# Kernel tuning notes

Measured on AMD Instinct MI355X. Metric: run time of the kernel, lower is better.

## Reference

```python
import jax, jax.numpy as jnp
import numpy as np
from jax import lax

E, H, D = 1024, 16, 64          # embed_dim, num_heads, head_dim
B, T = 8, 64                    # batch, decode chunk
KV = 4096                       # kv_seq_len -> cache capacity 2*KV
START = 4096                    # start_pos (prefill already filled cache[:START])
THETA = 10000.0


def setup_inputs() -> dict:
    key = jax.random.key(0)
    kx, kck, kcv, kq, kk, kv, ko = jax.random.split(key, 7)
    s = 0.02
    return {
        "x": jax.random.normal(kx, (B, T, E), jnp.float32),
        "cache_keys": jax.random.normal(kck, (B, 2 * KV, H, D), jnp.float32),
        "cache_values": jax.random.normal(kcv, (B, 2 * KV, H, D), jnp.float32),
        "Wq": jax.random.normal(kq, (E, E), jnp.float32) * s,
        "Wk": jax.random.normal(kk, (E, E), jnp.float32) * s,
        "Wv": jax.random.normal(kv, (E, E), jnp.float32) * s,
        "Wo": jax.random.normal(ko, (E, E), jnp.float32) * s,
        "start_pos": START,
    }


def _rope_bug_faithful(x, start_pos):
    # x: (B, T, H, Dd). The source helper unpacks (B,H,T,D)=x.shape on a (B,T,H,D)
    # tensor, so rotation angles are indexed by HEAD index (positions
    # start_pos..start_pos+H-1) and broadcast over the time axis. Reproduced exactly.
    Bn, Tn, Hn, Dd = x.shape
    dh = Dd // 2
    inv_freq = 1.0 / (THETA ** (jnp.arange(dh, dtype=jnp.float32) / dh))
    pos = jnp.arange(Hn, dtype=jnp.float32) + jnp.float32(start_pos)  # (H,)
    ang = pos[:, None] * inv_freq[None, :]                            # (H, dh)
    cos = jnp.cos(ang)[None, None]                                    # (1,1,H,dh)
    sin = jnp.sin(ang)[None, None]
    xr = x.reshape(Bn, Tn, Hn, dh, 2)
    x0, x1 = xr[..., 0], xr[..., 1]
    o0 = x0 * cos - x1 * sin
    o1 = x0 * sin + x1 * cos
    return jnp.stack([o0, o1], axis=-1).reshape(Bn, Tn, Hn, Dd)


def reference(x, cache_keys, cache_values, Wq, Wk, Wv, Wo, start_pos):
    Bn, Tn, C = x.shape
    Hn, Dd = cache_keys.shape[2], cache_keys.shape[3]
    scale = 1.0 / np.sqrt(Dd).astype(np.float32)
    end = start_pos + Tn

    q = (x @ Wq).reshape(Bn, Tn, Hn, Dd)
    k = (x @ Wk).reshape(Bn, Tn, Hn, Dd)
    v = (x @ Wv).reshape(Bn, Tn, Hn, Dd)

    q = _rope_bug_faithful(q, start_pos)
    k = _rope_bug_faithful(k, start_pos)

    # cache append at dynamic offset (detached in source)
    ck = lax.dynamic_update_slice_in_dim(cache_keys, lax.stop_gradient(k), start_pos, axis=1)
    cv = lax.dynamic_update_slice_in_dim(cache_values, lax.stop_gradient(v), start_pos, axis=1)
    k_full = lax.stop_gradient(ck[:, :end])  # (B, S, H, D), S = end
    v_full = lax.stop_gradient(cv[:, :end])

    qh = q.transpose(0, 2, 1, 3)        # (B,H,T,D)
    kh = k_full.transpose(0, 2, 1, 3)   # (B,H,S,D)
    vh = v_full.transpose(0, 2, 1, 3)

    scores = jnp.einsum("bhtd,bhsd->bhts", qh, kh) * scale  # (B,H,T,S)
    i = jnp.arange(Tn)[:, None]
    j = jnp.arange(end)[None, :]
    allowed = j <= (start_pos + i)      # intended causal mask over cache span
    neg = jnp.finfo(scores.dtype).min
    scores = jnp.where(allowed[None, None], scores, neg)
    attn = jax.nn.softmax(scores, axis=-1)
    ctx = jnp.einsum("bhts,bhsd->bhtd", attn, vh)
    out = ctx.transpose(0, 2, 1, 3).reshape(Bn, Tn, C) @ Wo
    return out
```

## Files before the change

kernel.cpp:

```cpp
#include <hip/hip_runtime.h>
#include <hip/hip_bf16.h>
#include <math.h>

typedef __attribute__((ext_vector_type(8))) __bf16 bf16x8;
typedef __attribute__((ext_vector_type(4))) __bf16 bf16x4;
typedef __attribute__((ext_vector_type(4))) float f32x4;

#define EE 1024
#define HH 16
#define DD 64
#define BB 8
#define TT 64
#define NSPLIT 8

__device__ __forceinline__ f32x4 mfma16(bf16x8 a, bf16x8 b, f32x4 c) {
    return __builtin_amdgcn_mfma_f32_16x16x32_bf16(a, b, c, 0, 0, 0);
}

__global__ __launch_bounds__(256) void k_prep(const float* __restrict__ Wq, const float* __restrict__ Wk,
                                              const float* __restrict__ Wv, const float* __restrict__ Wo,
                                              const float* __restrict__ x, const int* __restrict__ sp_ptr,
                                              __bf16* __restrict__ WT, __bf16* __restrict__ xb,
                                              float* __restrict__ cs, float* __restrict__ sn) {
    __shared__ float tile[64][68];
    int bid = blockIdx.x;
    int tid = threadIdx.x;
    if (bid < 1024) {
        int w = bid >> 8, tl = bid & 255;
        int k0 = (tl >> 4) * 64, n0 = (tl & 15) * 64;
        const float* W = (w == 0) ? Wq : (w == 1) ? Wk : (w == 2) ? Wv : Wo;
#pragma unroll
        for (int p = 0; p < 4; ++p) {
            int idx = p * 256 + tid;
            int r = idx >> 4, c4 = (idx & 15) * 4;
            float4 f = *(const float4*)&W[(size_t)(k0 + r) * EE + n0 + c4];
            *(float4*)&tile[r][c4] = f;
        }
        __syncthreads();
        __bf16* out = WT + (size_t)w * EE * EE;
#pragma unroll
        for (int p = 0; p < 2; ++p) {
            int q = p * 256 + tid;
            int r = q >> 3, c8 = (q & 7) * 8;
            bf16x8 v;
#pragma unroll
            for (int j = 0; j < 8; ++j) v[j] = (__bf16)tile[c8 + j][r];
            *(bf16x8*)&out[(size_t)(n0 + r) * EE + k0 + c8] = v;
        }
    } else if (bid < 1280) {
        int i = ((bid - 1024) * 256 + tid) * 8;
        float4 a = *(const float4*)&x[i];
        float4 b = *(const float4*)&x[i + 4];
        bf16x8 v;
        v[0] = (__bf16)a.x; v[1] = (__bf16)a.y; v[2] = (__bf16)a.z; v[3] = (__bf16)a.w;
        v[4] = (__bf16)b.x; v[5] = (__bf16)b.y; v[6] = (__bf16)b.z; v[7] = (__bf16)b.w;
        *(bf16x8*)&xb[i] = v;
    } else {
        int sp = sp_ptr[0];
#pragma unroll
        for (int q = 0; q < 2; ++q) {
            int i = q * 256 + tid;
            int h = i >> 5, p = i & 31;
            double inv = 1.0 / pow(10000.0, (double)p / 32.0);
            double ang = (double)(sp + h) * inv;
            cs[i] = (float)cos(ang);
            sn[i] = (float)sin(ang);
        }
    }
}

__global__ __launch_bounds__(256) void k_qkv(const __bf16* __restrict__ xb, const __bf16* __restrict__ WT,
                                             const float* __restrict__ cs, const float* __restrict__ sn,
                                             __bf16* __restrict__ qws, __bf16* __restrict__ knew,
                                             __bf16* __restrict__ vnew) {
    __shared__ __bf16 a_lds[64][72];
    __shared__ __bf16 b_lds[64][72];
    int xcd = blockIdx.x & 7, idx = blockIdx.x >> 3;
    int bn = xcd * 6 + idx % 6;
    int bm = idx / 6;
    int wsel = bn >> 4;
    int n0 = (bn & 15) * 64;
    int m0 = bm * 64;
    const __bf16* Wt = WT + (size_t)wsel * EE * EE;
    int tid = threadIdx.x;
    int wv = tid >> 6, lane = tid & 63;
    int l16 = lane & 15, lhi = lane >> 4;
    int r0 = tid >> 3, c8 = (tid & 7) * 8;

    f32x4 acc[4];
#pragma unroll
    for (int f = 0; f < 4; ++f) acc[f] = (f32x4){0.f, 0.f, 0.f, 0.f};

    bf16x8 ar0 = *(const bf16x8*)&xb[(size_t)(m0 + r0) * EE + c8];
    bf16x8 ar1 = *(const bf16x8*)&xb[(size_t)(m0 + 32 + r0) * EE + c8];
    bf16x8 br0 = *(const bf16x8*)&Wt[(size_t)(n0 + r0) * EE + c8];
    bf16x8 br1 = *(const bf16x8*)&Wt[(size_t)(n0 + 32 + r0) * EE + c8];

    for (int kt = 0; kt < 16; ++kt) {
        __syncthreads();
        *(bf16x8*)&a_lds[r0][c8] = ar0;
        *(bf16x8*)&a_lds[32 + r0][c8] = ar1;
        *(bf16x8*)&b_lds[r0][c8] = br0;
        *(bf16x8*)&b_lds[32 + r0][c8] = br1;
        if (kt < 15) {
            int ko = (kt + 1) * 64;
            ar0 = *(const bf16x8*)&xb[(size_t)(m0 + r0) * EE + ko + c8];
            ar1 = *(const bf16x8*)&xb[(size_t)(m0 + 32 + r0) * EE + ko + c8];
            br0 = *(const bf16x8*)&Wt[(size_t)(n0 + r0) * EE + ko + c8];
            br1 = *(const bf16x8*)&Wt[(size_t)(n0 + 32 + r0) * EE + ko + c8];
        }
        __syncthreads();
        bf16x8 a0 = *(bf16x8*)&a_lds[wv * 16 + l16][lhi * 8];
        bf16x8 a1 = *(bf16x8*)&a_lds[wv * 16 + l16][32 + lhi * 8];
#pragma unroll
        for (int f = 0; f < 4; ++f) {
            bf16x8 b0 = *(bf16x8*)&b_lds[f * 16 + l16][lhi * 8];
            bf16x8 b1 = *(bf16x8*)&b_lds[f * 16 + l16][32 + lhi * 8];
            acc[f] = mfma16(a0, b0, acc[f]);
            acc[f] = mfma16(a1, b1, acc[f]);
        }
    }
    __bf16* dst = (wsel == 0) ? qws : (wsel == 1) ? knew : vnew;
#pragma unroll
    for (int f = 0; f < 4; ++f) {
#pragma unroll
        for (int r = 0; r < 4; ++r) {
            float v = acc[f][r];
            int row = m0 + wv * 16 + lhi * 4 + r;
            int ng = n0 + f * 16 + l16;
            int h = ng >> 6, d = ng & 63;
            float o = v;
            if (wsel < 2) {
                float other = __shfl_xor(v, 1);
                int pp = d >> 1;
                float c = cs[h * 32 + pp], s = sn[h * 32 + pp];
                o = ((d & 1) == 0) ? (v * c - other * s) : (other * s + v * c);
            }
            int b = row >> 6, t = row & 63;
            dst[((size_t)((b * HH + h) * TT + t)) * DD + d] = (__bf16)o;
        }
    }
}

__global__ __launch_bounds__(256, 4) void k_attn(const __bf16* __restrict__ qws, const __bf16* __restrict__ knew,
                                                 const __bf16* __restrict__ vnew,
                                                 const float* __restrict__ ck, const float* __restrict__ cv,
                                                 __bf16* __restrict__ Opart, float2* __restrict__ mlpart) {
    __shared__ __bf16 k_lds[64][72];
    __shared__ __bf16 vT_lds[64][68];
    __shared__ __bf16 p_lds[64][72];
    int bh = blockIdx.x >> 3, split = blockIdx.x & 7;
    int b = bh >> 4, h = bh & 15;
    int tid = threadIdx.x, wv = tid >> 6, lane = tid & 63;
    int l16 = lane & 15, lhi = lane >> 4;
    int g = tid >> 4, m4 = (tid & 15) * 4;

    bf16x8 qf0, qf1;
    {
        const __bf16* qp = qws + ((size_t)bh * TT + (wv * 16 + l16)) * DD;
        qf0 = *(const bf16x8*)&qp[lhi * 8];
        qf1 = *(const bf16x8*)&qp[32 + lhi * 8];
    }
    f32x4 acc[4];
#pragma unroll
    for (int f = 0; f < 4; ++f) acc[f] = (f32x4){0.f, 0.f, 0.f, 0.f};
    float m[4], l[4];
#pragma unroll
    for (int r = 0; r < 4; ++r) { m[r] = -1e30f; l[r] = 0.f; }

    const float* ckb = ck + (size_t)b * 8192 * EE + h * DD;
    const float* cvb = cv + (size_t)b * 8192 * EE + h * DD;
    int s0 = split * 512;

    auto compute = [&](bool mask) {
        f32x4 sf[4];
#pragma unroll
        for (int f = 0; f < 4; ++f) {
            f32x4 z = (f32x4){0.f, 0.f, 0.f, 0.f};
            bf16x8 b0 = *(bf16x8*)&k_lds[f * 16 + l16][lhi * 8];
            bf16x8 b1 = *(bf16x8*)&k_lds[f * 16 + l16][32 + lhi * 8];
            z = mfma16(qf0, b0, z);
            z = mfma16(qf1, b1, z);
            sf[f] = z;
        }
#pragma unroll
        for (int f = 0; f < 4; ++f) {
#pragma unroll
            for (int r = 0; r < 4; ++r) {
                float sv = sf[f][r] * 0.125f;
                if (mask) {
                    int t_row = wv * 16 + lhi * 4 + r;
                    int s_loc = f * 16 + l16;
                    if (s_loc > t_row) sv = -1e30f;
                }
                sf[f][r] = sv;
            }
        }
        float mt[4];
#pragma unroll
        for (int r = 0; r < 4; ++r)
            mt[r] = fmaxf(fmaxf(sf[0][r], sf[1][r]), fmaxf(sf[2][r], sf[3][r]));
#pragma unroll
        for (int off = 1; off < 16; off <<= 1) {
#pragma unroll
            for (int r = 0; r < 4; ++r) mt[r] = fmaxf(mt[r], __shfl_xor(mt[r], off));
        }
        float fac[4];
#pragma unroll
        for (int r = 0; r < 4; ++r) {
            float mn = fmaxf(m[r], mt[r]);
            fac[r] = __expf(m[r] - mn);
            m[r] = mn;
        }
        float ladd[4] = {0.f, 0.f, 0.f, 0.f};
#pragma unroll
        for (int f = 0; f < 4; ++f) {
#pragma unroll
            for (int r = 0; r < 4; ++r) {
                float pv = __expf(sf[f][r] - m[r]);
                sf[f][r] = pv;
                ladd[r] += pv;
            }
        }
#pragma unroll
        for (int off = 1; off < 16; off <<= 1) {
#pragma unroll
            for (int r = 0; r < 4; ++r) ladd[r] += __shfl_xor(ladd[r], off);
        }
#pragma unroll
        for (int r = 0; r < 4; ++r) l[r] = l[r] * fac[r] + ladd[r];
#pragma unroll
        for (int f = 0; f < 4; ++f)
#pragma unroll
            for (int r = 0; r < 4; ++r) acc[f][r] *= fac[r];
#pragma unroll
        for (int f = 0; f < 4; ++f)
#pragma unroll
            for (int r = 0; r < 4; ++r)
                p_lds[wv * 16 + lhi * 4 + r][f * 16 + l16] = (__bf16)sf[f][r];
        bf16x8 pa0 = *(bf16x8*)&p_lds[wv * 16 + l16][lhi * 8];
        bf16x8 pa1 = *(bf16x8*)&p_lds[wv * 16 + l16][32 + lhi * 8];
#pragma unroll
        for (int f = 0; f < 4; ++f) {
            bf16x8 v0 = *(bf16x8*)&vT_lds[f * 16 + l16][lhi * 8];
            bf16x8 v1 = *(bf16x8*)&vT_lds[f * 16 + l16][32 + lhi * 8];
            acc[f] = mfma16(pa0, v0, acc[f]);
            acc[f] = mfma16(pa1, v1, acc[f]);
        }
    };

    f32x4 kreg[4], vreg[4];
#pragma unroll
    for (int p = 0; p < 4; ++p)
        kreg[p] = *(const f32x4*)&ckb[(size_t)(s0 + p * 16 + g) * EE + m4];
#pragma unroll
    for (int i = 0; i < 4; ++i)
        vreg[i] = *(const f32x4*)&cvb[(size_t)(s0 + 4 * g + i) * EE + m4];

    for (int it = 0; it < 8; ++it) {
#pragma unroll
        for (int p = 0; p < 4; ++p) {
            bf16x4 k4 = { (__bf16)kreg[p][0], (__bf16)kreg[p][1], (__bf16)kreg[p][2], (__bf16)kreg[p][3] };
            *(bf16x4*)&k_lds[p * 16 + g][m4] = k4;
        }
#pragma unroll
        for (int j = 0; j < 4; ++j) {
            bf16x4 tv = { (__bf16)vreg[0][j], (__bf16)vreg[1][j], (__bf16)vreg[2][j], (__bf16)vreg[3][j] };
            *(bf16x4*)&vT_lds[m4 + j][4 * g] = tv;
        }
        if (it < 7) {
            int sb = s0 + (it + 1) * 64;
#pragma unroll
            for (int p = 0; p < 4; ++p)
                kreg[p] = *(const f32x4*)&ckb[(size_t)(sb + p * 16 + g) * EE + m4];
#pragma unroll
            for (int i = 0; i < 4; ++i)
                vreg[i] = *(const f32x4*)&cvb[(size_t)(sb + 4 * g + i) * EE + m4];
        }
        __syncthreads();
        compute(false);
        __syncthreads();
    }

    if (split == 7) {
#pragma unroll
        for (int p = 0; p < 2; ++p) {
            int idx = p * 256 + tid;
            int r = idx >> 3, c8 = (idx & 7) * 8;
            *(bf16x8*)&k_lds[r][c8] = *(const bf16x8*)&knew[((size_t)bh * TT + r) * DD + c8];
            bf16x8 vf = *(const bf16x8*)&vnew[((size_t)bh * TT + r) * DD + c8];
#pragma unroll
            for (int j = 0; j < 8; ++j) vT_lds[c8 + j][r] = vf[j];
        }
        __syncthreads();
        compute(true);
    }

#pragma unroll
    for (int f = 0; f < 4; ++f)
#pragma unroll
        for (int r = 0; r < 4; ++r) {
            int t = wv * 16 + lhi * 4 + r;
            int d = f * 16 + l16;
            Opart[(((size_t)split * 128 + bh) * TT + t) * DD + d] = (__bf16)acc[f][r];
        }
    if (l16 == 0) {
#pragma unroll
        for (int r = 0; r < 4; ++r) {
            int t = wv * 16 + lhi * 4 + r;
            mlpart[((size_t)split * 128 + bh) * TT + t] = make_float2(m[r], l[r]);
        }
    }
}

__global__ __launch_bounds__(256) void k_combine(const __bf16* __restrict__ Opart, const float2* __restrict__ mlpart,
                                                 __bf16* __restrict__ ctxb) {
    int idx = blockIdx.x * 256 + threadIdx.x;
    int d = idx & 63, t = (idx >> 6) & 63, bh = idx >> 12;
    float ms[NSPLIT], ls[NSPLIT];
    float mg = -1e30f;
#pragma unroll
    for (int s = 0; s < NSPLIT; ++s) {
        float2 ml = mlpart[((size_t)s * 128 + bh) * TT + t];
        ms[s] = ml.x; ls[s] = ml.y;
        mg = fmaxf(mg, ms[s]);
    }
    float den = 0.f, num = 0.f;
#pragma unroll
    for (int s = 0; s < NSPLIT; ++s) {
        float w = __expf(ms[s] - mg);
        den += ls[s] * w;
        num += (float)Opart[(((size_t)s * 128 + bh) * TT + t) * DD + d] * w;
    }
    float ctx = num / den;
    int b = bh >> 4, hh = bh & 15;
    ctxb[(size_t)(b * TT + t) * EE + hh * DD + d] = (__bf16)ctx;
}

__global__ __launch_bounds__(256) void k_oproj(const __bf16* __restrict__ ctxb, const __bf16* __restrict__ WoT,
                                               float* __restrict__ out) {
    __shared__ __bf16 a_lds[64][72];
    __shared__ __bf16 b_lds[64][72];
    int xcd = blockIdx.x & 7, idx = blockIdx.x >> 3;
    int bn = xcd * 2 + (idx & 1);
    int bm = idx >> 1;
    int n0 = bn * 64, m0 = bm * 64;
    int tid = threadIdx.x;
    int wv = tid >> 6, lane = tid & 63;
    int l16 = lane & 15, lhi = lane >> 4;
    int r0 = tid >> 3, c8 = (tid & 7) * 8;
    f32x4 acc[4];
#pragma unroll
    for (int f = 0; f < 4; ++f) acc[f] = (f32x4){0.f, 0.f, 0.f, 0.f};

    bf16x8 ar0 = *(const bf16x8*)&ctxb[(size_t)(m0 + r0) * EE + c8];
    bf16x8 ar1 = *(const bf16x8*)&ctxb[(size_t)(m0 + 32 + r0) * EE + c8];
    bf16x8 br0 = *(const bf16x8*)&WoT[(size_t)(n0 + r0) * EE + c8];
    bf16x8 br1 = *(const bf16x8*)&WoT[(size_t)(n0 + 32 + r0) * EE + c8];

    for (int kt = 0; kt < 16; ++kt) {
        __syncthreads();
        *(bf16x8*)&a_lds[r0][c8] = ar0;
        *(bf16x8*)&a_lds[32 + r0][c8] = ar1;
        *(bf16x8*)&b_lds[r0][c8] = br0;
        *(bf16x8*)&b_lds[32 + r0][c8] = br1;
        if (kt < 15) {
            int ko = (kt + 1) * 64;
            ar0 = *(const bf16x8*)&ctxb[(size_t)(m0 + r0) * EE + ko + c8];
            ar1 = *(const bf16x8*)&ctxb[(size_t)(m0 + 32 + r0) * EE + ko + c8];
            br0 = *(const bf16x8*)&WoT[(size_t)(n0 + r0) * EE + ko + c8];
            br1 = *(const bf16x8*)&WoT[(size_t)(n0 + 32 + r0) * EE + ko + c8];
        }
        __syncthreads();
        bf16x8 a0 = *(bf16x8*)&a_lds[wv * 16 + l16][lhi * 8];
        bf16x8 a1 = *(bf16x8*)&a_lds[wv * 16 + l16][32 + lhi * 8];
#pragma unroll
        for (int f = 0; f < 4; ++f) {
            bf16x8 b0 = *(bf16x8*)&b_lds[f * 16 + l16][lhi * 8];
            bf16x8 b1 = *(bf16x8*)&b_lds[f * 16 + l16][32 + lhi * 8];
            acc[f] = mfma16(a0, b0, acc[f]);
            acc[f] = mfma16(a1, b1, acc[f]);
        }
    }
#pragma unroll
    for (int f = 0; f < 4; ++f)
#pragma unroll
        for (int r = 0; r < 4; ++r) {
            int row = m0 + wv * 16 + lhi * 4 + r;
            out[(size_t)row * EE + n0 + f * 16 + l16] = acc[f][r];
        }
}

extern "C" void kernel_launch(void* const* d_in, const int* in_sizes, int n_in,
                              void* d_out, int out_size, void* d_ws, size_t ws_size,
                              hipStream_t stream) {
    const float* x  = (const float*)d_in[0];
    const float* ck = (const float*)d_in[1];
    const float* cv = (const float*)d_in[2];
    const float* Wq = (const float*)d_in[3];
    const float* Wk = (const float*)d_in[4];
    const float* Wv = (const float*)d_in[5];
    const float* Wo = (const float*)d_in[6];
    const int* sp   = (const int*)d_in[7];
    float* out = (float*)d_out;

    char* p = (char*)d_ws;
    float* cs = (float*)p;              p += 2048;
    float* sn = (float*)p;              p += 2048;
    __bf16* xb = (__bf16*)p;            p += (size_t)512 * 1024 * 2;
    __bf16* WT = (__bf16*)p;            p += (size_t)4 * 1024 * 1024 * 2;
    __bf16* qws = (__bf16*)p;           p += (size_t)524288 * 2;
    __bf16* knew = (__bf16*)p;          p += (size_t)524288 * 2;
    __bf16* vnew = (__bf16*)p;          p += (size_t)524288 * 2;
    __bf16* Opart = (__bf16*)p;         p += (size_t)NSPLIT * 128 * 64 * 64 * 2;
    float2* mlpart = (float2*)p;        p += (size_t)NSPLIT * 8192 * 8;
    __bf16* ctxb = (__bf16*)p;          p += (size_t)524288 * 2;

    k_prep<<<1281, 256, 0, stream>>>(Wq, Wk, Wv, Wo, x, sp, WT, xb, cs, sn);
    k_qkv<<<384, 256, 0, stream>>>(xb, WT, cs, sn, qws, knew, vnew);
    k_attn<<<BB * HH * NSPLIT, 256, 0, stream>>>(qws, knew, vnew, ck, cv, Opart, mlpart);
    k_combine<<<2048, 256, 0, stream>>>(Opart, mlpart, ctxb);
    k_oproj<<<128, 256, 0, stream>>>(ctxb, WT + (size_t)3 * 1024 * 1024, out);
}
```

Baseline: 87.35 us.

## Fuse fp32-to-bf16 weight/input conversion and RoPE tables into GEMM kernels

Removes the separate prep kernel that transposed and converted all four weight matrices and x to bf16 and built the RoPE cos/sin tables. The QKV and output-projection GEMMs now read fp32 x and W directly, convert and transpose into LDS on the fly, and compute the per-head RoPE factors in shared memory. M tiles grow from 64 to 128 rows, halving the grid sizes. This saves a launch and an extra pass over 16MB of weights, but each GEMM now loads twice the bytes per element and runs on fewer blocks. RoPE angles also drop from double to float precision.

```diff
diff --git a/kernel.cpp b/kernel.cpp
--- a/kernel.cpp
+++ b/kernel.cpp
@@ -17,127 +17,111 @@
     return __builtin_amdgcn_mfma_f32_16x16x32_bf16(a, b, c, 0, 0, 0);
 }
 
-__global__ __launch_bounds__(256) void k_prep(const float* __restrict__ Wq, const float* __restrict__ Wk,
-                                              const float* __restrict__ Wv, const float* __restrict__ Wo,
-                                              const float* __restrict__ x, const int* __restrict__ sp_ptr,
-                                              __bf16* __restrict__ WT, __bf16* __restrict__ xb,
-                                              float* __restrict__ cs, float* __restrict__ sn) {
-    __shared__ float tile[64][68];
-    int bid = blockIdx.x;
-    int tid = threadIdx.x;
-    if (bid < 1024) {
-        int w = bid >> 8, tl = bid & 255;
-        int k0 = (tl >> 4) * 64, n0 = (tl & 15) * 64;
-        const float* W = (w == 0) ? Wq : (w == 1) ? Wk : (w == 2) ? Wv : Wo;
-#pragma unroll
-        for (int p = 0; p < 4; ++p) {
-            int idx = p * 256 + tid;
-            int r = idx >> 4, c4 = (idx & 15) * 4;
-            float4 f = *(const float4*)&W[(size_t)(k0 + r) * EE + n0 + c4];
-            *(float4*)&tile[r][c4] = f;
-        }
-        __syncthreads();
-        __bf16* out = WT + (size_t)w * EE * EE;
-#pragma unroll
-        for (int p = 0; p < 2; ++p) {
-            int q = p * 256 + tid;
-            int r = q >> 3, c8 = (q & 7) * 8;
-            bf16x8 v;
-#pragma unroll
-            for (int j = 0; j < 8; ++j) v[j] = (__bf16)tile[c8 + j][r];
-            *(bf16x8*)&out[(size_t)(n0 + r) * EE + k0 + c8] = v;
-        }
-    } else if (bid < 1280) {
-        int i = ((bid - 1024) * 256 + tid) * 8;
-        float4 a = *(const float4*)&x[i];
-        float4 b = *(const float4*)&x[i + 4];
-        bf16x8 v;
-        v[0] = (__bf16)a.x; v[1] = (__bf16)a.y; v[2] = (__bf16)a.z; v[3] = (__bf16)a.w;
-        v[4] = (__bf16)b.x; v[5] = (__bf16)b.y; v[6] = (__bf16)b.z; v[7] = (__bf16)b.w;
-        *(bf16x8*)&xb[i] = v;
-    } else {
-        int sp = sp_ptr[0];
-#pragma unroll
-        for (int q = 0; q < 2; ++q) {
-            int i = q * 256 + tid;
-            int h = i >> 5, p = i & 31;
-            double inv = 1.0 / pow(10000.0, (double)p / 32.0);
-            double ang = (double)(sp + h) * inv;
-            cs[i] = (float)cos(ang);
-            sn[i] = (float)sin(ang);
-        }
-    }
-}
-
-__global__ __launch_bounds__(256) void k_qkv(const __bf16* __restrict__ xb, const __bf16* __restrict__ WT,
-                                             const float* __restrict__ cs, const float* __restrict__ sn,
+__global__ __launch_bounds__(256) void k_qkv(const float* __restrict__ x, const float* __restrict__ Wq,
+                                             const float* __restrict__ Wk, const float* __restrict__ Wv,
+                                             const int* __restrict__ sp_ptr,
                                              __bf16* __restrict__ qws, __bf16* __restrict__ knew,
                                              __bf16* __restrict__ vnew) {
-    __shared__ __bf16 a_lds[64][72];
+    __shared__ __bf16 a_lds[128][72];
     __shared__ __bf16 b_lds[64][72];
+    __shared__ float cs_l[32], sn_l[32];
     int xcd = blockIdx.x & 7, idx = blockIdx.x >> 3;
     int bn = xcd * 6 + idx % 6;
     int bm = idx / 6;
     int wsel = bn >> 4;
     int n0 = (bn & 15) * 64;
-    int m0 = bm * 64;
-    const __bf16* Wt = WT + (size_t)wsel * EE * EE;
+    int m0 = bm * 128;
+    const float* W = (wsel == 0) ? Wq : (wsel == 1) ? Wk : Wv;
     int tid = threadIdx.x;
     int wv = tid >> 6, lane = tid & 63;
     int l16 = lane & 15, lhi = lane >> 4;
-    int r0 = tid >> 3, c8 = (tid & 7) * 8;
-
-    f32x4 acc[4];
-#pragma unroll
-    for (int f = 0; f < 4; ++f) acc[f] = (f32x4){0.f, 0.f, 0.f, 0.f};
-
-    bf16x8 ar0 = *(const bf16x8*)&xb[(size_t)(m0 + r0) * EE + c8];
-    bf16x8 ar1 = *(const bf16x8*)&xb[(size_t)(m0 + 32 + r0) * EE + c8];
-    bf16x8 br0 = *(const bf16x8*)&Wt[(size_t)(n0 + r0) * EE + c8];
-    bf16x8 br1 = *(const bf16x8*)&Wt[(size_t)(n0 + 32 + r0) * EE + c8];
+    int g = tid >> 4, m4 = (tid & 15) * 4;
+
+    f32x4 acc[2][4];
+#pragma unroll
+    for (int im = 0; im < 2; ++im)
+#pragma unroll
+        for (int f = 0; f < 4; ++f) acc[im][f] = (f32x4){0.f, 0.f, 0.f, 0.f};
+
+    f32x4 areg[8], breg[4];
+#pragma unroll
+    for (int p = 0; p < 8; ++p)
+        areg[p] = *(const f32x4*)&x[(size_t)(m0 + p * 16 + g) * EE + m4];
+#pragma unroll
+    for (int i = 0; i < 4; ++i)
+        breg[i] = *(const f32x4*)&W[(size_t)(4 * g + i) * EE + n0 + m4];
+
+    if (tid < 32) {
+        int h = bn & 15;
+        int sp = sp_ptr[0];
+        float invf = powf(10000.0f, -(float)tid / 32.0f);
+        float ang = (float)(sp + h) * invf;
+        float s, c;
+        sincosf(ang, &s, &c);
+        cs_l[tid] = c;
+        sn_l[tid] = s;
+    }
 
     for (int kt = 0; kt < 16; ++kt) {
         __syncthreads();
-        *(bf16x8*)&a_lds[r0][c8] = ar0;
-        *(bf16x8*)&a_lds[32 + r0][c8] = ar1;
-        *(bf16x8*)&b_lds[r0][c8] = br0;
-        *(bf16x8*)&b_lds[32 + r0][c8] = br1;
+#pragma unroll
+        for (int p = 0; p < 8; ++p) {
+            bf16x4 a4 = { (__bf16)areg[p][0], (__bf16)areg[p][1], (__bf16)areg[p][2], (__bf16)areg[p][3] };
+            *(bf16x4*)&a_lds[p * 16 + g][m4] = a4;
+        }
+#pragma unroll
+        for (int j = 0; j < 4; ++j) {
+            bf16x4 t4 = { (__bf16)breg[0][j], (__bf16)breg[1][j], (__bf16)breg[2][j], (__bf16)breg[3][j] };
+            *(bf16x4*)&b_lds[m4 + j][4 * g] = t4;
+        }
         if (kt < 15) {
             int ko = (kt + 1) * 64;
-            ar0 = *(const bf16x8*)&xb[(size_t)(m0 + r0) * EE + ko + c8];
-            ar1 = *(const bf16x8*)&xb[(size_t)(m0 + 32 + r0) * EE + ko + c8];
-            br0 = *(const bf16x8*)&Wt[(size_t)(n0 + r0) * EE + ko + c8];
-            br1 = *(const bf16x8*)&Wt[(size_t)(n0 + 32 + r0) * EE + ko + c8];
-        }
-        __syncthreads();
-        bf16x8 a0 = *(bf16x8*)&a_lds[wv * 16 + l16][lhi * 8];
-        bf16x8 a1 = *(bf16x8*)&a_lds[wv * 16 + l16][32 + lhi * 8];
+#pragma unroll
+            for (int p = 0; p < 8; ++p)
+                areg[p] = *(const f32x4*)&x[(size_t)(m0 + p * 16 + g) * EE + ko + m4];
+#pragma unroll
+            for (int i = 0; i < 4; ++i)
+                breg[i] = *(const f32x4*)&W[(size_t)(ko + 4 * g + i) * EE + n0 + m4];
+        }
+        __syncthreads();
+        bf16x8 a0[2], a1[2];
+#pragma unroll
+        for (int im = 0; im < 2; ++im) {
+            a0[im] = *(bf16x8*)&a_lds[wv * 32 + im * 16 + l16][lhi * 8];
+            a1[im] = *(bf16x8*)&a_lds[wv * 32 + im * 16 + l16][32 + lhi * 8];
+        }
 #pragma unroll
         for (int f = 0; f < 4; ++f) {
             bf16x8 b0 = *(bf16x8*)&b_lds[f * 16 + l16][lhi * 8];
             bf16x8 b1 = *(bf16x8*)&b_lds[f * 16 + l16][32 + lhi * 8];
-            acc[f] = mfma16(a0, b0, acc[f]);
-            acc[f] = mfma16(a1, b1, acc[f]);
+#pragma unroll
+            for (int im = 0; im < 2; ++im) {
+                acc[im][f] = mfma16(a0[im], b0, acc[im][f]);
+                acc[im][f] = mfma16(a1[im], b1, acc[im][f]);
+            }
         }
     }
     __bf16* dst = (wsel == 0) ? qws : (wsel == 1) ? knew : vnew;
-#pragma unroll
-    for (int f = 0; f < 4; ++f) {
-#pragma unroll
-        for (int r = 0; r < 4; ++r) {
-            float v = acc[f][r];
-            int row = m0 + wv * 16 + lhi * 4 + r;
-            int ng = n0 + f * 16 + l16;
-            int h = ng >> 6, d = ng & 63;
-            float o = v;
-            if (wsel < 2) {
-                float other = __shfl_xor(v, 1);
-                int pp = d >> 1;
-                float c = cs[h * 32 + pp], s = sn[h * 32 + pp];
-                o = ((d & 1) == 0) ? (v * c - other * s) : (other * s + v * c);
-            }
-            int b = row >> 6, t = row & 63;
-            dst[((size_t)((b * HH + h) * TT + t)) * DD + d] = (__bf16)o;
+    int h = bn & 15;
+#pragma unroll
+    for (int im = 0; im < 2; ++im) {
+#pragma unroll
+        for (int f = 0; f < 4; ++f) {
+#pragma unroll
+            for (int r = 0; r < 4; ++r) {
+                float v = acc[im][f][r];
+                int row = m0 + wv * 32 + im * 16 + lhi * 4 + r;
+                int d = f * 16 + l16;
+                float o = v;
+                if (wsel < 2) {
+                    float other = __shfl_xor(v, 1);
+                    int pp = d >> 1;
+                    float c = cs_l[pp], s = sn_l[pp];
+                    o = ((d & 1) == 0) ? (v * c - other * s) : (other * s + v * c);
+                }
+                int b = row >> 6, t = row & 63;
+                dst[((size_t)((b * HH + h) * TT + t)) * DD + d] = (__bf16)o;
+            }
         }
     }
 }
@@ -337,58 +321,80 @@
     ctxb[(size_t)(b * TT + t) * EE + hh * DD + d] = (__bf16)ctx;
 }
 
-__global__ __launch_bounds__(256) void k_oproj(const __bf16* __restrict__ ctxb, const __bf16* __restrict__ WoT,
+__global__ __launch_bounds__(256) void k_oproj(const __bf16* __restrict__ ctxb, const float* __restrict__ Wo,
                                                float* __restrict__ out) {
-    __shared__ __bf16 a_lds[64][72];
+    __shared__ __bf16 a_lds[128][72];
     __shared__ __bf16 b_lds[64][72];
     int xcd = blockIdx.x & 7, idx = blockIdx.x >> 3;
     int bn = xcd * 2 + (idx & 1);
     int bm = idx >> 1;
-    int n0 = bn * 64, m0 = bm * 64;
+    int n0 = bn * 64, m0 = bm * 128;
     int tid = threadIdx.x;
     int wv = tid >> 6, lane = tid & 63;
     int l16 = lane & 15, lhi = lane >> 4;
-    int r0 = tid >> 3, c8 = (tid & 7) * 8;
-    f32x4 acc[4];
-#pragma unroll
-    for (int f = 0; f < 4; ++f) acc[f] = (f32x4){0.f, 0.f, 0.f, 0.f};
-
-    bf16x8 ar0 = *(const bf16x8*)&ctxb[(size_t)(m0 + r0) * EE + c8];
-    bf16x8 ar1 = *(const bf16x8*)&ctxb[(size_t)(m0 + 32 + r0) * EE + c8];
-    bf16x8 br0 = *(const bf16x8*)&WoT[(size_t)(n0 + r0) * EE + c8];
-    bf16x8 br1 = *(const bf16x8*)&WoT[(size_t)(n0 + 32 + r0) * EE + c8];
+    int g = tid >> 4, m4 = (tid & 15) * 4;
+    int q8 = tid >> 3, c8 = (tid & 7) * 8;
+    f32x4 acc[2][4];
+#pragma unroll
+    for (int im = 0; im < 2; ++im)
+#pragma unroll
+        for (int f = 0; f < 4; ++f) acc[im][f] = (f32x4){0.f, 0.f, 0.f, 0.f};
+
+    bf16x8 areg[4];
+    f32x4 breg[4];
+#pragma unroll
+    for (int p = 0; p < 4; ++p)
+        areg[p] = *(const bf16x8*)&ctxb[(size_t)(m0 + p * 32 + q8) * EE + c8];
+#pragma unroll
+    for (int i = 0; i < 4; ++i)
+        breg[i] = *(const f32x4*)&Wo[(size_t)(4 * g + i) * EE + n0 + m4];
 
     for (int kt = 0; kt < 16; ++kt) {
         __syncthreads();
-        *(bf16x8*)&a_lds[r0][c8] = ar0;
-        *(bf16x8*)&a_lds[32 + r0][c8] = ar1;
-        *(bf16x8*)&b_lds[r0][c8] = br0;
-        *(bf16x8*)&b_lds[32 + r0][c8] = br1;
+#pragma unroll
+        for (int p = 0; p < 4; ++p)
+            *(bf16x8*)&a_lds[p * 32 + q8][c8] = areg[p];
+#pragma unroll
+        for (int j = 0; j < 4; ++j) {
+            bf16x4 t4 = { (__bf16)breg[0][j], (__bf16)breg[1][j], (__bf16)breg[2][j], (__bf16)breg[3][j] };
+            *(bf16x4*)&b_lds[m4 + j][4 * g] = t4;
+        }
         if (kt < 15) {
             int ko = (kt + 1) * 64;
-            ar0 = *(const bf16x8*)&ctxb[(size_t)(m0 + r0) * EE + ko + c8];
-            ar1 = *(const bf16x8*)&ctxb[(size_t)(m0 + 32 + r0) * EE + ko + c8];
-            br0 = *(const bf16x8*)&WoT[(size_t)(n0 + r0) * EE + ko + c8];
-            br1 = *(const bf16x8*)&WoT[(size_t)(n0 + 32 + r0) * EE + ko + c8];
-        }
-        __syncthreads();
-        bf16x8 a0 = *(bf16x8*)&a_lds[wv * 16 + l16][lhi * 8];
-        bf16x8 a1 = *(bf16x8*)&a_lds[wv * 16 + l16][32 + lhi * 8];
+#pragma unroll
+            for (int p = 0; p < 4; ++p)
+                areg[p] = *(const bf16x8*)&ctxb[(size_t)(m0 + p * 32 + q8) * EE + ko + c8];
+#pragma unroll
+            for (int i = 0; i < 4; ++i)
+                breg[i] = *(const f32x4*)&Wo[(size_t)(ko + 4 * g + i) * EE + n0 + m4];
+        }
+        __syncthreads();
+        bf16x8 a0[2], a1[2];
+#pragma unroll
+        for (int im = 0; im < 2; ++im) {
+            a0[im] = *(bf16x8*)&a_lds[wv * 32 + im * 16 + l16][lhi * 8];
+            a1[im] = *(bf16x8*)&a_lds[wv * 32 + im * 16 + l16][32 + lhi * 8];
+        }
 #pragma unroll
         for (int f = 0; f < 4; ++f) {
             bf16x8 b0 = *(bf16x8*)&b_lds[f * 16 + l16][lhi * 8];
             bf16x8 b1 = *(bf16x8*)&b_lds[f * 16 + l16][32 + lhi * 8];
-            acc[f] = mfma16(a0, b0, acc[f]);
-            acc[f] = mfma16(a1, b1, acc[f]);
-        }
-    }
-#pragma unroll
-    for (int f = 0; f < 4; ++f)
-#pragma unroll
-        for (int r = 0; r < 4; ++r) {
-            int row = m0 + wv * 16 + lhi * 4 + r;
-            out[(size_t)row * EE + n0 + f * 16 + l16] = acc[f][r];
-        }
+#pragma unroll
+            for (int im = 0; im < 2; ++im) {
+                acc[im][f] = mfma16(a0[im], b0, acc[im][f]);
+                acc[im][f] = mfma16(a1[im], b1, acc[im][f]);
+            }
+        }
+    }
+#pragma unroll
+    for (int im = 0; im < 2; ++im)
+#pragma unroll
+        for (int f = 0; f < 4; ++f)
+#pragma unroll
+            for (int r = 0; r < 4; ++r) {
+                int row = m0 + wv * 32 + im * 16 + lhi * 4 + r;
+                out[(size_t)row * EE + n0 + f * 16 + l16] = acc[im][f][r];
+            }
 }
 
 extern "C" void kernel_launch(void* const* d_in, const int* in_sizes, int n_in,
@@ -405,10 +411,6 @@
     float* out = (float*)d_out;
 
     char* p = (char*)d_ws;
-    float* cs = (float*)p;              p += 2048;
-    float* sn = (float*)p;              p += 2048;
-    __bf16* xb = (__bf16*)p;            p += (size_t)512 * 1024 * 2;
-    __bf16* WT = (__bf16*)p;            p += (size_t)4 * 1024 * 1024 * 2;
     __bf16* qws = (__bf16*)p;           p += (size_t)524288 * 2;
     __bf16* knew = (__bf16*)p;          p += (size_t)524288 * 2;
     __bf16* vnew = (__bf16*)p;          p += (size_t)524288 * 2;
@@ -416,9 +418,8 @@
     float2* mlpart = (float2*)p;        p += (size_t)NSPLIT * 8192 * 8;
     __bf16* ctxb = (__bf16*)p;          p += (size_t)524288 * 2;
 
-    k_prep<<<1281, 256, 0, stream>>>(Wq, Wk, Wv, Wo, x, sp, WT, xb, cs, sn);
-    k_qkv<<<384, 256, 0, stream>>>(xb, WT, cs, sn, qws, knew, vnew);
+    k_qkv<<<192, 256, 0, stream>>>(x, Wq, Wk, Wv, sp, qws, knew, vnew);
     k_attn<<<BB * HH * NSPLIT, 256, 0, stream>>>(qws, knew, vnew, ck, cv, Opart, mlpart);
     k_combine<<<2048, 256, 0, stream>>>(Opart, mlpart, ctxb);
-    k_oproj<<<128, 256, 0, stream>>>(ctxb, WT + (size_t)3 * 1024 * 1024, out);
-}
+    k_oproj<<<64, 256, 0, stream>>>(ctxb, Wo, out);
+}
```

After: 92.22 us. +5.6%, slower.
